# Performance work log

Measured on AMD Instinct MI355X. Metric: run time of the kernel, lower is better.

Reference implementation:

```python
import jax, jax.numpy as jnp
import numpy as np

N = 50000   # nodes
E = 300000  # directed edges (~Delaunay mesh, degree 6)
H = 128     # hidden_size
TW = 5      # time_window
P = 3       # process_steps
NODE_IN = 9
EDGE_IN = 4
LN_EPS = 1e-5


def _ln(x, g, b):
    m = jnp.mean(x, axis=-1, keepdims=True)
    v = jnp.var(x, axis=-1, keepdims=True)
    return (x - m) * jax.lax.rsqrt(v + LN_EPS) * g + b


def _mlp_ln(x, w1, b1, w2, b2, g, bb):
    # Linear -> ReLU -> Linear -> LayerNorm (matches MLP(..., layer_norm=True))
    h = jax.nn.relu(x @ w1 + b1)
    return _ln(h @ w2 + b2, g, bb)


def setup_inputs() -> dict:
    key = jax.random.key(0)
    ks = iter(jax.random.split(key, 64))
    def nrm(shape):
        return jax.random.normal(next(ks), shape, jnp.float32)
    def lin(fi, fo, stack=None):
        sh = (fi, fo) if stack is None else (stack, fi, fo)
        return nrm(sh) / np.sqrt(fi)
    inp = {}
    inp["temperature"] = nrm((N,))
    inp["temperature_prev"] = nrm((N,))
    inp["heat_source"] = nrm((N,))
    inp["heat_source_prev"] = nrm((N,))
    inp["heat_source_next"] = nrm((N, TW))
    inp["mesh_pos"] = jax.random.uniform(next(ks), (N, 2), jnp.float32)
    inp["edge_index"] = jax.random.randint(next(ks), (2, E), 0, N, jnp.int32)
    # Normalizer params (running mean/std)
    inp["node_norm_mean"] = jnp.zeros((NODE_IN,), jnp.float32)
    inp["node_norm_std"] = jnp.ones((NODE_IN,), jnp.float32)
    inp["edge_norm_mean"] = jnp.zeros((EDGE_IN,), jnp.float32)
    inp["edge_norm_std"] = jnp.ones((EDGE_IN,), jnp.float32)
    # node encoder
    inp["ne_w1"] = lin(NODE_IN, H); inp["ne_b1"] = jnp.zeros((H,), jnp.float32)
    inp["ne_w2"] = lin(H, H);       inp["ne_b2"] = jnp.zeros((H,), jnp.float32)
    inp["ne_g"] = jnp.ones((H,), jnp.float32); inp["ne_be"] = jnp.zeros((H,), jnp.float32)
    # edge encoder
    inp["ee_w1"] = lin(EDGE_IN, H); inp["ee_b1"] = jnp.zeros((H,), jnp.float32)
    inp["ee_w2"] = lin(H, H);       inp["ee_b2"] = jnp.zeros((H,), jnp.float32)
    inp["ee_g"] = jnp.ones((H,), jnp.float32); inp["ee_be"] = jnp.zeros((H,), jnp.float32)
    # processors (stacked over P steps): edge_mlp in=3H, node_mlp in=2H
    inp["pe_w1"] = lin(3 * H, H, P); inp["pe_b1"] = jnp.zeros((P, H), jnp.float32)
    inp["pe_w2"] = lin(H, H, P);     inp["pe_b2"] = jnp.zeros((P, H), jnp.float32)
    inp["pe_g"] = jnp.ones((P, H), jnp.float32); inp["pe_be"] = jnp.zeros((P, H), jnp.float32)
    inp["pn_w1"] = lin(2 * H, H, P); inp["pn_b1"] = jnp.zeros((P, H), jnp.float32)
    inp["pn_w2"] = lin(H, H, P);     inp["pn_b2"] = jnp.zeros((P, H), jnp.float32)
    inp["pn_g"] = jnp.ones((P, H), jnp.float32); inp["pn_be"] = jnp.zeros((P, H), jnp.float32)
    # decoder (Conv1d kernel_size=1 == per-node Linear), Swish in between
    inp["dec_w1"] = lin(H, H // 2); inp["dec_b1"] = jnp.zeros((H // 2,), jnp.float32)
    inp["dec_w2"] = lin(H // 2, TW); inp["dec_b2"] = jnp.zeros((TW,), jnp.float32)
    return inp


def reference(temperature, temperature_prev, heat_source, heat_source_prev,
              heat_source_next, mesh_pos, edge_index,
              node_norm_mean, node_norm_std, edge_norm_mean, edge_norm_std,
              ne_w1, ne_b1, ne_w2, ne_b2, ne_g, ne_be,
              ee_w1, ee_b1, ee_w2, ee_b2, ee_g, ee_be,
              pe_w1, pe_b1, pe_w2, pe_b2, pe_g, pe_be,
              pn_w1, pn_b1, pn_w2, pn_b2, pn_g, pn_be,
              dec_w1, dec_b1, dec_w2, dec_b2):
    u = temperature
    # node features: [u, u_dot, q, q_dot, q_next]  -> [N, 9]
    x = jnp.concatenate([
        u[:, None], (u - temperature_prev)[:, None],
        heat_source[:, None], (heat_source - heat_source_prev)[:, None],
        heat_source_next], axis=-1)
    s, r = edge_index[0], edge_index[1]  # senders (source j), receivers (target i)
    rel = mesh_pos[s] - mesh_pos[r]                       # [E, 2]
    dist = jnp.linalg.norm(rel, axis=-1, keepdims=True)   # [E, 1]
    relt = (u[s] - u[r])[:, None]                         # [E, 1]
    e = jnp.concatenate([rel, dist, relt], axis=-1)       # [E, 4]

    xh = _mlp_ln((x - node_norm_mean) / node_norm_std, ne_w1, ne_b1, ne_w2, ne_b2, ne_g, ne_be)
    eh = _mlp_ln((e - edge_norm_mean) / edge_norm_std, ee_w1, ee_b1, ee_w2, ee_b2, ee_g, ee_be)

    n_nodes = xh.shape[0]
    for i in range(P):
        xs, xr = xh[s], xh[r]  # x_j = x[source], x_i = x[target]
        # message: edge_mlp(cat[x_i, x_j, e]) then scatter-add at target index
        msg = _mlp_ln(jnp.concatenate([xr, xs, eh], axis=-1),
                      pe_w1[i], pe_b1[i], pe_w2[i], pe_b2[i], pe_g[i], pe_be[i])
        aggr = jax.ops.segment_sum(msg, r, num_segments=n_nodes)
        # node update + residual
        new_x = _mlp_ln(jnp.concatenate([aggr, xh], axis=-1),
                        pn_w1[i], pn_b1[i], pn_w2[i], pn_b2[i], pn_g[i], pn_be[i]) + xh
        # edge update (note row/col ordering differs from message) + residual
        new_e = _mlp_ln(jnp.concatenate([xs, xr, eh], axis=-1),
                        pe_w1[i], pe_b1[i], pe_w2[i], pe_b2[i], pe_g[i], pe_be[i]) + eh
        xh, eh = new_x, new_e

    # decoder: 1x1 convs == per-node linears, Swish(beta=1) activation
    h = xh @ dec_w1 + dec_b1
    h = h * jax.nn.sigmoid(h)
    delta = (h @ dec_w2 + dec_b2).reshape(-1, TW)
    dt = jnp.arange(1, TW + 1, dtype=delta.dtype)
    return dt[None, :] * delta
```

## Files before the change

### kernel.cpp

```cpp
#include <hip/hip_runtime.h>
#include <stdint.h>

typedef unsigned short u16;
typedef __attribute__((ext_vector_type(8))) short bf16x8_t;
typedef __attribute__((ext_vector_type(4))) float f32x4_t;

__device__ __forceinline__ float bl(u16 x) {
  union { unsigned u; float f; } c; c.u = ((unsigned)x) << 16; return c.f;
}
__device__ __forceinline__ u16 fb(float x) {
  union { float f; unsigned u; } c; c.f = x;
  unsigned r = c.u + 0x7fffu + ((c.u >> 16) & 1u);
  return (u16)(r >> 16);
}

__global__ void sentinel_kernel(float* out, int n) {
  int i = blockIdx.x * 256 + threadIdx.x;
  if (i < n) out[i] = 12345.f;
}

struct TSeg { const float* src; u16* dst; };
struct TArgs { TSeg s[23]; };
__global__ void transpose_w(TArgs a) {
  __shared__ u16 sT[128][132];
  const float* src = a.s[blockIdx.x].src;
  u16* dst = a.s[blockIdx.x].dst;
  for (int e = threadIdx.x; e < 16384; e += 256) {
    int k = e >> 7, n = e & 127;
    sT[n][k] = fb(src[e]);
  }
  __syncthreads();
  for (int e = threadIdx.x; e < 16384; e += 256) {
    int n = e >> 7, k = e & 127;
    dst[e] = sT[n][k];
  }
}

__global__ void zero_i32(int* p, int n) {
  int i = blockIdx.x * 256 + threadIdx.x;
  if (i < n) p[i] = 0;
}
__global__ void deg_count(const int* __restrict__ ei, int* __restrict__ cnt, int E) {
  int e = blockIdx.x * 256 + threadIdx.x;
  if (e < E) atomicAdd(&cnt[ei[E + e]], 1);
}
__global__ void scan1(const int* __restrict__ cnt, int* __restrict__ part,
                      int* __restrict__ bsum, int N) {
  __shared__ int s[256];
  int i = blockIdx.x * 256 + threadIdx.x;
  s[threadIdx.x] = (i < N) ? cnt[i] : 0;
  __syncthreads();
#pragma unroll
  for (int o = 1; o < 256; o <<= 1) {
    int t = (threadIdx.x >= o) ? s[threadIdx.x - o] : 0;
    __syncthreads();
    s[threadIdx.x] += t;
    __syncthreads();
  }
  if (i < N) part[i] = s[threadIdx.x];
  if (threadIdx.x == 255) bsum[blockIdx.x] = s[255];
}
__global__ void scan2(int* bsum, int nb) {
  __shared__ int s[256];
  __shared__ int carry;
  if (threadIdx.x == 0) carry = 0;
  __syncthreads();
  for (int base = 0; base < nb; base += 256) {
    int i = base + threadIdx.x;
    int v = (i < nb) ? bsum[i] : 0;
    s[threadIdx.x] = v;
    __syncthreads();
#pragma unroll
    for (int o = 1; o < 256; o <<= 1) {
      int t = (threadIdx.x >= o) ? s[threadIdx.x - o] : 0;
      __syncthreads();
      s[threadIdx.x] += t;
      __syncthreads();
    }
    int exc = s[threadIdx.x] - v + carry;
    if (i < nb) bsum[i] = exc;
    __syncthreads();
    if (threadIdx.x == 255) carry += s[255];
    __syncthreads();
  }
}
__global__ void scan3(const int* __restrict__ part, const int* __restrict__ bsum,
                      int* __restrict__ start, int N) {
  int i = blockIdx.x * 256 + threadIdx.x;
  if (i < N) start[i + 1] = part[i] + bsum[i >> 8];
  if (i == 0) start[0] = 0;
}
__global__ void fill_slot(const int* __restrict__ ei, int* __restrict__ cnt2,
                          const int* __restrict__ start, int* __restrict__ sortedS,
                          int* __restrict__ sortedR, int E) {
  int e = blockIdx.x * 256 + threadIdx.x;
  if (e >= E) return;
  int s = ei[e], r = ei[E + e];
  int p = atomicAdd(&cnt2[r], 1);
  int slot = start[r] + p;
  sortedS[slot] = s;
  sortedR[slot] = r;
}

__global__ void node_feat_kernel(const float* __restrict__ t, const float* __restrict__ tp,
                                 const float* __restrict__ q, const float* __restrict__ qp,
                                 const float* __restrict__ qn, const float* __restrict__ nm,
                                 const float* __restrict__ ns, float* __restrict__ nfeat,
                                 int n_nodes) {
  int n = blockIdx.x * 256 + threadIdx.x;
  if (n >= n_nodes) return;
  float u = t[n];
  float x[9];
  x[0] = u; x[1] = u - tp[n];
  float hq = q[n];
  x[2] = hq; x[3] = hq - qp[n];
#pragma unroll
  for (int j = 0; j < 5; ++j) x[4 + j] = qn[n * 5 + j];
#pragma unroll
  for (int k = 0; k < 9; ++k) nfeat[n * 9 + k] = (x[k] - nm[k]) / ns[k];
}

__global__ void edge_feat_kernel(const int* __restrict__ sArr, const int* __restrict__ rArr,
                                 const float* __restrict__ mp, const float* __restrict__ u,
                                 const float* __restrict__ em, const float* __restrict__ es,
                                 float* __restrict__ efeat, int n_edges) {
  int e = blockIdx.x * 256 + threadIdx.x;
  if (e >= n_edges) return;
  int s = sArr[e], r = rArr[e];
  float rx = mp[s * 2] - mp[r * 2];
  float ry = mp[s * 2 + 1] - mp[r * 2 + 1];
  float d = sqrtf(rx * rx + ry * ry);
  float rt = u[s] - u[r];
  float x[4] = {rx, ry, d, rt};
#pragma unroll
  for (int k = 0; k < 4; ++k) efeat[e * 4 + k] = (x[k] - em[k]) / es[k];
}

template <int K>
__global__ __launch_bounds__(256, 2) void encode_fused(
    const float* __restrict__ feat, const float* __restrict__ w1f, const float* __restrict__ b1f,
    const u16* __restrict__ wt2, const float* __restrict__ b2, const float* __restrict__ gg,
    const float* __restrict__ bb, u16* __restrict__ out, int M) {
  __shared__ float sW1[K * 128];
  __shared__ float sB1[128];
  __shared__ u16 sH[64][136];
  const int tid = threadIdx.x;
  const int wave = tid >> 6, lane = tid & 63;
  const int q = lane >> 4, l16 = lane & 15;
  const int m0 = blockIdx.x * 64;
  const int rowb = wave * 16 + q * 4;
  const int arow = m0 + wave * 16 + l16;
  const int arc = arow < M ? arow : M - 1;

  for (int i = tid; i < K * 128; i += 256) sW1[i] = w1f[i];
  if (tid < 128) sB1[tid] = b1f[tid];
  __syncthreads();

  float fr[K];
#pragma unroll
  for (int k = 0; k < K; ++k) fr[k] = feat[(size_t)arc * K + k];

  f32x4_t acc[8];
#pragma unroll
  for (int b = 0; b < 8; ++b) acc[b] = (f32x4_t){0.f, 0.f, 0.f, 0.f};
#pragma unroll
  for (int kk = 0; kk < 4; ++kk) {
    union { u16 u[8]; bf16x8_t v; } cv;
#pragma unroll
    for (int j = 0; j < 8; ++j) {
      int col = kk * 32 + q * 8 + j;
      float h = sB1[col];
#pragma unroll
      for (int k = 0; k < K; ++k) h += fr[k] * sW1[k * 128 + col];
      cv.u[j] = fb(h > 0.f ? h : 0.f);
    }
#pragma unroll
    for (int nt = 0; nt < 8; ++nt) {
      bf16x8_t bfv = *(const bf16x8_t*)(wt2 + (size_t)(nt * 16 + l16) * 128 + kk * 32 + q * 8);
      acc[nt] = __builtin_amdgcn_mfma_f32_16x16x32_bf16(cv.v, bfv, acc[nt], 0, 0, 0);
    }
  }

  float bcol[8], gcol[8], becol[8];
#pragma unroll
  for (int nt = 0; nt < 8; ++nt) {
    bcol[nt] = b2[nt * 16 + l16];
    gcol[nt] = gg[nt * 16 + l16];
    becol[nt] = bb[nt * 16 + l16];
  }
  float s[4] = {0, 0, 0, 0}, ss[4] = {0, 0, 0, 0};
#pragma unroll
  for (int r = 0; r < 4; ++r)
#pragma unroll
    for (int nt = 0; nt < 8; ++nt) {
      float v = acc[nt][r] + bcol[nt];
      s[r] += v;
      ss[r] += v * v;
    }
#pragma unroll
  for (int r = 0; r < 4; ++r) {
#pragma unroll
    for (int m = 1; m <= 8; m <<= 1) {
      s[r] += __shfl_xor(s[r], m, 64);
      ss[r] += __shfl_xor(ss[r], m, 64);
    }
  }
#pragma unroll
  for (int r = 0; r < 4; ++r) {
    float mean = s[r] * (1.f / 128.f);
    float var = fmaxf(ss[r] * (1.f / 128.f) - mean * mean, 0.f);
    float rstd = rsqrtf(var + 1e-5f);
#pragma unroll
    for (int nt = 0; nt < 8; ++nt) {
      float v = (acc[nt][r] + bcol[nt] - mean) * rstd * gcol[nt] + becol[nt];
      sH[rowb + r][nt * 16 + l16] = fb(v);
    }
  }
  __syncthreads();
#pragma unroll
  for (int it = 0; it < 4; ++it) {
    int lin = it * 256 + tid;
    int row = lin >> 4, ch = (lin & 15) * 8;
    int grow = m0 + row;
    if (grow >= M) continue;
    *(uint4*)(out + (size_t)grow * 128 + ch) = *(uint4*)(&sH[row][ch]);
  }
}

__global__ __launch_bounds__(256, 2) void gemm64_2w(
    const u16* __restrict__ A, const u16* __restrict__ WT0, const u16* __restrict__ WT1,
    u16* __restrict__ out0, u16* __restrict__ out1, float* __restrict__ aggr, int M) {
  __shared__ u16 sO0[64][136];
  __shared__ u16 sO1[64][136];
  const int tid = threadIdx.x;
  const int wave = tid >> 6, lane = tid & 63;
  const int q = lane >> 4, l16 = lane & 15;
  const int m0 = blockIdx.x * 64;
  int arow = m0 + wave * 16 + l16;
  if (arow >= M) arow = M - 1;

  {
    float4 z = make_float4(0.f, 0.f, 0.f, 0.f);
#pragma unroll
    for (int it = 0; it < 8; ++it) {
      int lin = it * 256 + tid;
      int row = lin >> 5, c4 = (lin & 31) * 4;
      int grow = m0 + row;
      if (grow < M) *(float4*)(aggr + (size_t)grow * 128 + c4) = z;
    }
  }

  f32x4_t a0[8], a1[8];
#pragma unroll
  for (int b = 0; b < 8; ++b) {
    a0[b] = (f32x4_t){0.f, 0.f, 0.f, 0.f};
    a1[b] = (f32x4_t){0.f, 0.f, 0.f, 0.f};
  }
#pragma unroll 2
  for (int kk = 0; kk < 4; ++kk) {
    bf16x8_t af = *(const bf16x8_t*)(A + (size_t)arow * 128 + kk * 32 + q * 8);
#pragma unroll
    for (int nt = 0; nt < 8; ++nt) {
      bf16x8_t b0 = *(const bf16x8_t*)(WT0 + (size_t)(nt * 16 + l16) * 128 + kk * 32 + q * 8);
      bf16x8_t b1v = *(const bf16x8_t*)(WT1 + (size_t)(nt * 16 + l16) * 128 + kk * 32 + q * 8);
      a0[nt] = __builtin_amdgcn_mfma_f32_16x16x32_bf16(af, b0, a0[nt], 0, 0, 0);
      a1[nt] = __builtin_amdgcn_mfma_f32_16x16x32_bf16(af, b1v, a1[nt], 0, 0, 0);
    }
  }
  const int rowb = wave * 16 + q * 4;
#pragma unroll
  for (int r = 0; r < 4; ++r)
#pragma unroll
    for (int nt = 0; nt < 8; ++nt) {
      sO0[rowb + r][nt * 16 + l16] = fb(a0[nt][r]);
      sO1[rowb + r][nt * 16 + l16] = fb(a1[nt][r]);
    }
  __syncthreads();
#pragma unroll
  for (int it = 0; it < 4; ++it) {
    int lin = it * 256 + tid;
    int row = lin >> 4, ch = (lin & 15) * 8;
    int grow = m0 + row;
    if (grow >= M) continue;
    *(uint4*)(out0 + (size_t)grow * 128 + ch) = *(uint4*)(&sO0[row][ch]);
    *(uint4*)(out1 + (size_t)grow * 128 + ch) = *(uint4*)(&sO1[row][ch]);
  }
}

__global__ __launch_bounds__(256, 2) void node_fused_2w(
    u16* __restrict__ xh, float* __restrict__ aggr, const u16* __restrict__ wtA,
    const u16* __restrict__ wtB, const float* __restrict__ b1, const u16* __restrict__ wt2,
    const float* __restrict__ b2, const float* __restrict__ gg, const float* __restrict__ bb,
    const u16* __restrict__ wtA2, const u16* __restrict__ wtB2, u16* __restrict__ xhA,
    u16* __restrict__ xhB, int M) {
  __shared__ u16 sH[64][136];
  __shared__ u16 sO1[64][136];
  const int tid = threadIdx.x;
  const int wave = tid >> 6, lane = tid & 63;
  const int q = lane >> 4, l16 = lane & 15;
  const int m0 = blockIdx.x * 64;
  const int rowb = wave * 16 + q * 4;
  const int arow = m0 + wave * 16 + l16;
  const int arc = arow < M ? arow : M - 1;

  bf16x8_t xf[4], af_[4];
#pragma unroll
  for (int kk = 0; kk < 4; ++kk) {
    xf[kk] = *(const bf16x8_t*)(xh + (size_t)arc * 128 + kk * 32 + q * 8);
    const float* ap = aggr + (size_t)arc * 128 + kk * 32 + q * 8;
    union { u16 u[8]; bf16x8_t v; } cv;
#pragma unroll
    for (int j = 0; j < 8; ++j) cv.u[j] = fb(ap[j]);
    af_[kk] = cv.v;
  }

  f32x4_t acc[8];
#pragma unroll
  for (int b = 0; b < 8; ++b) acc[b] = (f32x4_t){0.f, 0.f, 0.f, 0.f};
#pragma unroll
  for (int kk = 0; kk < 4; ++kk) {
#pragma unroll
    for (int nt = 0; nt < 8; ++nt) {
      bf16x8_t bA = *(const bf16x8_t*)(wtA + (size_t)(nt * 16 + l16) * 128 + kk * 32 + q * 8);
      bf16x8_t bB = *(const bf16x8_t*)(wtB + (size_t)(nt * 16 + l16) * 128 + kk * 32 + q * 8);
      acc[nt] = __builtin_amdgcn_mfma_f32_16x16x32_bf16(af_[kk], bA, acc[nt], 0, 0, 0);
      acc[nt] = __builtin_amdgcn_mfma_f32_16x16x32_bf16(xf[kk], bB, acc[nt], 0, 0, 0);
    }
  }
  float bcol1[8];
#pragma unroll
  for (int nt = 0; nt < 8; ++nt) bcol1[nt] = b1[nt * 16 + l16];
#pragma unroll
  for (int r = 0; r < 4; ++r)
#pragma unroll
    for (int nt = 0; nt < 8; ++nt) {
      float v = acc[nt][r] + bcol1[nt];
      sH[rowb + r][nt * 16 + l16] = fb(v > 0.f ? v : 0.f);
    }
  __syncthreads();

  f32x4_t acc2[8];
#pragma unroll
  for (int b = 0; b < 8; ++b) acc2[b] = (f32x4_t){0.f, 0.f, 0.f, 0.f};
#pragma unroll
  for (int kk = 0; kk < 4; ++kk) {
    bf16x8_t afm = *(const bf16x8_t*)(&sH[wave * 16 + l16][kk * 32 + q * 8]);
#pragma unroll
    for (int nt = 0; nt < 8; ++nt) {
      bf16x8_t bfv = *(const bf16x8_t*)(wt2 + (size_t)(nt * 16 + l16) * 128 + kk * 32 + q * 8);
      acc2[nt] = __builtin_amdgcn_mfma_f32_16x16x32_bf16(afm, bfv, acc2[nt], 0, 0, 0);
    }
  }
  float bcol[8], gcol[8], becol[8];
#pragma unroll
  for (int nt = 0; nt < 8; ++nt) {
    bcol[nt] = b2[nt * 16 + l16];
    gcol[nt] = gg[nt * 16 + l16];
    becol[nt] = bb[nt * 16 + l16];
  }
  float s[4] = {0, 0, 0, 0}, ss[4] = {0, 0, 0, 0};
#pragma unroll
  for (int r = 0; r < 4; ++r)
#pragma unroll
    for (int nt = 0; nt < 8; ++nt) {
      float v = acc2[nt][r] + bcol[nt];
      s[r] += v;
      ss[r] += v * v;
    }
#pragma unroll
  for (int r = 0; r < 4; ++r) {
#pragma unroll
    for (int m = 1; m <= 8; m <<= 1) {
      s[r] += __shfl_xor(s[r], m, 64);
      ss[r] += __shfl_xor(ss[r], m, 64);
    }
  }
  __syncthreads();
#pragma unroll
  for (int r = 0; r < 4; ++r) {
    float mean = s[r] * (1.f / 128.f);
    float var = fmaxf(ss[r] * (1.f / 128.f) - mean * mean, 0.f);
    float rstd = rsqrtf(var + 1e-5f);
#pragma unroll
    for (int nt = 0; nt < 8; ++nt) {
      float v = (acc2[nt][r] + bcol[nt] - mean) * rstd * gcol[nt] + becol[nt];
      sH[rowb + r][nt * 16 + l16] = fb(v);
    }
  }
  __syncthreads();

  bf16x8_t nf[4];
#pragma unroll
  for (int kk = 0; kk < 4; ++kk) {
    u16 y8[8];
    *(uint4*)y8 = *(uint4*)(&sH[wave * 16 + l16][kk * 32 + q * 8]);
#pragma unroll
    for (int j = 0; j < 8; ++j) y8[j] = fb(bl(y8[j]) + bl((u16)xf[kk][j]));
    nf[kk] = *(bf16x8_t*)y8;
    if (arow < M)
      *(uint4*)(xh + (size_t)arow * 128 + kk * 32 + q * 8) = *(uint4*)y8;
  }

  if (wtA2 == nullptr) return;

  if (arow < M) {
    float4 z = make_float4(0.f, 0.f, 0.f, 0.f);
#pragma unroll
    for (int kk = 0; kk < 4; ++kk) {
      *(float4*)(aggr + (size_t)arow * 128 + kk * 32 + q * 8) = z;
      *(float4*)(aggr + (size_t)arow * 128 + kk * 32 + q * 8 + 4) = z;
    }
  }

  f32x4_t a0[8], a1[8];
#pragma unroll
  for (int b = 0; b < 8; ++b) {
    a0[b] = (f32x4_t){0.f, 0.f, 0.f, 0.f};
    a1[b] = (f32x4_t){0.f, 0.f, 0.f, 0.f};
  }
#pragma unroll
  for (int kk = 0; kk < 4; ++kk) {
#pragma unroll
    for (int nt = 0; nt < 8; ++nt) {
      bf16x8_t b0 = *(const bf16x8_t*)(wtA2 + (size_t)(nt * 16 + l16) * 128 + kk * 32 + q * 8);
      bf16x8_t b1v = *(const bf16x8_t*)(wtB2 + (size_t)(nt * 16 + l16) * 128 + kk * 32 + q * 8);
      a0[nt] = __builtin_amdgcn_mfma_f32_16x16x32_bf16(nf[kk], b0, a0[nt], 0, 0, 0);
      a1[nt] = __builtin_amdgcn_mfma_f32_16x16x32_bf16(nf[kk], b1v, a1[nt], 0, 0, 0);
    }
  }
  __syncthreads();
#pragma unroll
  for (int r = 0; r < 4; ++r)
#pragma unroll
    for (int nt = 0; nt < 8; ++nt) {
      sH[rowb + r][nt * 16 + l16] = fb(a0[nt][r]);
      sO1[rowb + r][nt * 16 + l16] = fb(a1[nt][r]);
    }
  __syncthreads();
#pragma unroll
  for (int it = 0; it < 4; ++it) {
    int lin = it * 256 + tid;
    int row = lin >> 4, ch = (lin & 15) * 8;
    int grow = m0 + row;
    if (grow >= M) continue;
    *(uint4*)(xhA + (size_t)grow * 128 + ch) = *(uint4*)(&sH[row][ch]);
    *(uint4*)(xhB + (size_t)grow * 128 + ch) = *(uint4*)(&sO1[row][ch]);
  }
}

template <bool CSR, bool LAST>
__global__ __launch_bounds__(256, 2) void edge_fused(
    u16* __restrict__ eh, const u16* __restrict__ xhA, const u16* __restrict__ xhB,
    const u16* __restrict__ wtC, const float* __restrict__ b1, const u16* __restrict__ wt2,
    const float* __restrict__ b2, const float* __restrict__ gg, const float* __restrict__ bb,
    const int* __restrict__ sArr, const int* __restrict__ rArr,
    const int* __restrict__ startp, float* __restrict__ aggr, int E) {
  __shared__ u16 sHm[64][136];
  __shared__ u16 sHe[LAST ? 1 : 64][136];
  __shared__ int sR[64];
  __shared__ float sB1[128];
  const int tid = threadIdx.x;
  const int wave = tid >> 6, lane = tid & 63;
  const int q = lane >> 4, l16 = lane & 15;
  const int m0 = blockIdx.x * 64;
  const int rowb = wave * 16 + q * 4;
  int arow = m0 + wave * 16 + l16;
  int arc = arow < E ? arow : E - 1;

  if (tid < 64) {
    int e = m0 + tid;
    sR[tid] = (e < E) ? rArr[e] : -1;
  }
  if (tid < 128) sB1[tid] = b1[tid];

  int psv[4], prv[4];
#pragma unroll
  for (int it = 0; it < 4; ++it) {
    int lin = it * 256 + tid;
    int ge = m0 + (lin >> 4);
    int gc = ge < E ? ge : E - 1;
    psv[it] = sArr[gc];
    prv[it] = rArr[gc];
  }

  bf16x8_t ehf[4];
#pragma unroll
  for (int kk = 0; kk < 4; ++kk)
    ehf[kk] = *(const bf16x8_t*)(eh + (size_t)arc * 128 + kk * 32 + q * 8);

  f32x4_t accC[8];
#pragma unroll
  for (int b = 0; b < 8; ++b) accC[b] = (f32x4_t){0.f, 0.f, 0.f, 0.f};
#pragma unroll
  for (int kk = 0; kk < 4; ++kk) {
#pragma unroll
    for (int nt = 0; nt < 8; ++nt) {
      bf16x8_t bfv = *(const bf16x8_t*)(wtC + (size_t)(nt * 16 + l16) * 128 + kk * 32 + q * 8);
      accC[nt] = __builtin_amdgcn_mfma_f32_16x16x32_bf16(ehf[kk], bfv, accC[nt], 0, 0, 0);
    }
  }
  __builtin_amdgcn_sched_barrier(0);

  uint4 pAr[4], pBs[4], pAs[4], pBr[4];
#pragma unroll
  for (int it = 0; it < 4; ++it) {
    int ch = ((it * 256 + tid) & 15) * 8;
    pAr[it] = *(const uint4*)(xhA + (size_t)prv[it] * 128 + ch);
    pBs[it] = *(const uint4*)(xhB + (size_t)psv[it] * 128 + ch);
    if constexpr (!LAST) {
      pAs[it] = *(const uint4*)(xhA + (size_t)psv[it] * 128 + ch);
      pBr[it] = *(const uint4*)(xhB + (size_t)prv[it] * 128 + ch);
    }
  }

#pragma unroll
  for (int r = 0; r < 4; ++r)
#pragma unroll
    for (int nt = 0; nt < 8; ++nt) sHm[rowb + r][nt * 16 + l16] = fb(accC[nt][r]);
  __syncthreads();

#pragma unroll
  for (int it = 0; it < 4; ++it) {
    int lin = it * 256 + tid;
    int row = lin >> 4, ch = (lin & 15) * 8;
    bool ok = (m0 + row) < E;
    u16 t8[8], ar[8], as_[8], br[8], bs[8], hm[8], he[8];
    *(uint4*)t8 = *(uint4*)(&sHm[row][ch]);
    *(uint4*)ar = pAr[it];
    *(uint4*)bs = pBs[it];
    if constexpr (!LAST) {
      *(uint4*)as_ = pAs[it];
      *(uint4*)br = pBr[it];
    }
#pragma unroll
    for (int j = 0; j < 8; ++j) {
      float t = bl(t8[j]) + sB1[ch + j];
      float vm = t + bl(ar[j]) + bl(bs[j]);
      hm[j] = (ok && vm > 0.f) ? fb(vm) : 0;
      if constexpr (!LAST) {
        float ve = t + bl(as_[j]) + bl(br[j]);
        he[j] = (ok && ve > 0.f) ? fb(ve) : 0;
      }
    }
    *(uint4*)(&sHm[row][ch]) = *(uint4*)hm;
    if constexpr (!LAST) *(uint4*)(&sHe[row][ch]) = *(uint4*)he;
  }
  __syncthreads();

  float bcol[8], gcol[8], becol[8];
#pragma unroll
  for (int nt = 0; nt < 8; ++nt) {
    bcol[nt] = b2[nt * 16 + l16];
    gcol[nt] = gg[nt * 16 + l16];
    becol[nt] = bb[nt * 16 + l16];
  }

  f32x4_t accM[8], accE[8];
#pragma unroll
  for (int b = 0; b < 8; ++b) {
    accM[b] = (f32x4_t){0.f, 0.f, 0.f, 0.f};
    accE[b] = (f32x4_t){0.f, 0.f, 0.f, 0.f};
  }
#pragma unroll
  for (int kk = 0; kk < 4; ++kk) {
    bf16x8_t afm = *(const bf16x8_t*)(&sHm[wave * 16 + l16][kk * 32 + q * 8]);
    bf16x8_t afe;
    if constexpr (!LAST) afe = *(const bf16x8_t*)(&sHe[wave * 16 + l16][kk * 32 + q * 8]);
#pragma unroll
    for (int nt = 0; nt < 8; ++nt) {
      bf16x8_t bfv = *(const bf16x8_t*)(wt2 + (size_t)(nt * 16 + l16) * 128 + kk * 32 + q * 8);
      accM[nt] = __builtin_amdgcn_mfma_f32_16x16x32_bf16(afm, bfv, accM[nt], 0, 0, 0);
      if constexpr (!LAST)
        accE[nt] = __builtin_amdgcn_mfma_f32_16x16x32_bf16(afe, bfv, accE[nt], 0, 0, 0);
    }
  }
  float sm[4] = {0, 0, 0, 0}, ssm[4] = {0, 0, 0, 0};
  float se[4] = {0, 0, 0, 0}, sse[4] = {0, 0, 0, 0};
#pragma unroll
  for (int r = 0; r < 4; ++r)
#pragma unroll
    for (int nt = 0; nt < 8; ++nt) {
      float vm = accM[nt][r] + bcol[nt];
      sm[r] += vm; ssm[r] += vm * vm;
      if constexpr (!LAST) {
        float ve = accE[nt][r] + bcol[nt];
        se[r] += ve; sse[r] += ve * ve;
      }
    }
#pragma unroll
  for (int r = 0; r < 4; ++r) {
#pragma unroll
    for (int m = 1; m <= 8; m <<= 1) {
      sm[r] += __shfl_xor(sm[r], m, 64);
      ssm[r] += __shfl_xor(ssm[r], m, 64);
      if constexpr (!LAST) {
        se[r] += __shfl_xor(se[r], m, 64);
        sse[r] += __shfl_xor(sse[r], m, 64);
      }
    }
  }

  if (!CSR) {
#pragma unroll
    for (int r = 0; r < 4; ++r) {
      int row = m0 + rowb + r;
      if (row >= E) continue;
      int rr = sR[rowb + r];
      float mean = sm[r] * (1.f / 128.f);
      float var = fmaxf(ssm[r] * (1.f / 128.f) - mean * mean, 0.f);
      float rstd = rsqrtf(var + 1e-5f);
#pragma unroll
      for (int nt = 0; nt < 8; ++nt) {
        float v = (accM[nt][r] + bcol[nt] - mean) * rstd * gcol[nt] + becol[nt];
        atomicAdd(&aggr[(size_t)rr * 128 + nt * 16 + l16], v);
      }
    }
  }

  __syncthreads();
#pragma unroll
  for (int r = 0; r < 4; ++r) {
    float meanM = sm[r] * (1.f / 128.f);
    float varM = fmaxf(ssm[r] * (1.f / 128.f) - meanM * meanM, 0.f);
    float rstdM = rsqrtf(varM + 1e-5f);
    if constexpr (!LAST) {
      float meanE = se[r] * (1.f / 128.f);
      float varE = fmaxf(sse[r] * (1.f / 128.f) - meanE * meanE, 0.f);
      float rstdE = rsqrtf(varE + 1e-5f);
#pragma unroll
      for (int nt = 0; nt < 8; ++nt) {
        float ve = (accE[nt][r] + bcol[nt] - meanE) * rstdE * gcol[nt] + becol[nt];
        sHe[rowb + r][nt * 16 + l16] = fb(ve);
      }
    }
    if (CSR) {
#pragma unroll
      for (int nt = 0; nt < 8; ++nt) {
        float vm = (accM[nt][r] + bcol[nt] - meanM) * rstdM * gcol[nt] + becol[nt];
        sHm[rowb + r][nt * 16 + l16] = fb(vm);
      }
    }
  }
  __syncthreads();

#pragma unroll
  for (int it = 0; it < 4; ++it) {
    int lin = it * 256 + tid;
    int row = lin >> 4, ch = (lin & 15) * 8;
    int grow = m0 + row;
    if (grow >= E) continue;
    if constexpr (!LAST) {
      u16 y8[8], e8[8];
      *(uint4*)y8 = *(uint4*)(&sHe[row][ch]);
      *(uint4*)e8 = *(const uint4*)(eh + (size_t)grow * 128 + ch);
#pragma unroll
      for (int j = 0; j < 8; ++j) y8[j] = fb(bl(y8[j]) + bl(e8[j]));
      *(uint4*)(eh + (size_t)grow * 128 + ch) = *(uint4*)y8;
    }

    if (CSR) {
      int rr = sR[row];
      if (rr < 0) continue;
      bool first = (row == 0) || (sR[row - 1] != rr);
      if (!first) continue;
      int gs = startp[rr], ge2 = startp[rr + 1];
      int le = ge2 - m0;
      if (le > 64) le = 64;
      float acc[8] = {0, 0, 0, 0, 0, 0, 0, 0};
      for (int i = row; i < le; ++i) {
        u16 m8[8];
        *(uint4*)m8 = *(uint4*)(&sHm[i][ch]);
#pragma unroll
        for (int j = 0; j < 8; ++j) acc[j] += bl(m8[j]);
      }
      if (gs >= m0 && ge2 <= m0 + 64) {
        *(float4*)(aggr + (size_t)rr * 128 + ch) = make_float4(acc[0], acc[1], acc[2], acc[3]);
        *(float4*)(aggr + (size_t)rr * 128 + ch + 4) =
            make_float4(acc[4], acc[5], acc[6], acc[7]);
      } else {
#pragma unroll
        for (int j = 0; j < 8; ++j) atomicAdd(&aggr[(size_t)rr * 128 + ch + j], acc[j]);
      }
    }
  }
}

__global__ void decoder_kernel(const u16* __restrict__ xh, const float* __restrict__ w1,
                               const float* __restrict__ b1, const float* __restrict__ w2,
                               const float* __restrict__ b2, float* __restrict__ out,
                               int n_nodes) {
  __shared__ float sx[4][128];
  int tid = threadIdx.x;
  int lw = tid >> 6, lane = tid & 63;
  int n0 = blockIdx.x * 4;
  for (int i = tid; i < 512; i += 256) {
    int nn = i >> 7, c = i & 127;
    int n = n0 + nn;
    sx[nn][c] = (n < n_nodes) ? bl(xh[(size_t)n * 128 + c]) : 0.f;
  }
  __syncthreads();
  int n = n0 + lw;
  float h = b1[lane];
#pragma unroll 16
  for (int k = 0; k < 128; ++k) h += sx[lw][k] * w1[k * 64 + lane];
  float hs = h * (1.f / (1.f + __expf(-h)));
  float d[5];
#pragma unroll
  for (int t = 0; t < 5; ++t) {
    float p = hs * w2[lane * 5 + t];
#pragma unroll
    for (int m = 1; m <= 32; m <<= 1) p += __shfl_xor(p, m, 64);
    d[t] = p;
  }
  if (lane == 0 && n < n_nodes) {
#pragma unroll
    for (int t = 0; t < 5; ++t)
      out[(size_t)n * 5 + t] = (float)(t + 1) * (d[t] + b2[t]);
  }
}

extern "C" void kernel_launch(void* const* d_in, const int* in_sizes, int n_in, void* d_out,
                              int out_size, void* d_ws, size_t ws_size, hipStream_t stream) {
  auto F = [&](int i) { return (const float*)d_in[i]; };
  const int* edge_index = (const int*)d_in[6];
  const int N_ = in_sizes[0];
  const int E_ = in_sizes[6] / 2;

  char* wsb = (char*)d_ws;
  size_t off = 0;
  auto alloc = [&](size_t bytes) -> char* {
    char* p = wsb + off;
    off += (bytes + 255) & ~(size_t)255;
    return p;
  };
  u16* xh = (u16*)alloc((size_t)N_ * 128 * 2);
  u16* xhA = (u16*)alloc((size_t)N_ * 128 * 2);
  u16* xhB = (u16*)alloc((size_t)N_ * 128 * 2);
  u16* ehP = (u16*)alloc((size_t)E_ * 128 * 2);
  float* aggr = (float*)alloc((size_t)N_ * 128 * 4);
  float* nfeat = (float*)xhA;
  float* efeat = (float*)xhB;
  u16* wne2T = (u16*)alloc(16384 * 2);
  u16* wee2T = (u16*)alloc(16384 * 2);
  u16* wpe1T = (u16*)alloc((size_t)9 * 16384 * 2);
  u16* wpe2T = (u16*)alloc((size_t)3 * 16384 * 2);
  u16* wpn1T = (u16*)alloc((size_t)6 * 16384 * 2);
  u16* wpn2T = (u16*)alloc((size_t)3 * 16384 * 2);

  const size_t base_off = off;
  int* startp = (int*)alloc((size_t)(N_ + 1) * 4);
  int* cntp = (int*)alloc((size_t)N_ * 4);
  int* partp = (int*)alloc((size_t)N_ * 4);
  int* bsump = (int*)alloc(((size_t)(N_ + 255) / 256) * 4 + 256);
  int* sortedS = (int*)alloc((size_t)E_ * 4);
  int* sortedR = (int*)alloc((size_t)E_ * 4);
  bool useCSR = (off <= ws_size);
  if (!useCSR) {
    off = base_off;
    if (off > ws_size) {
      sentinel_kernel<<<(out_size + 255) / 256, 256, 0, stream>>>((float*)d_out, out_size);
      return;
    }
  }

  TArgs ta;
  int ts = 0;
  ta.s[ts++] = {F(13), wne2T};
  ta.s[ts++] = {F(19), wee2T};
  for (int i = 0; i < 3; ++i)
    for (int b = 0; b < 3; ++b)
      ta.s[ts++] = {F(23) + (size_t)(i * 3 + b) * 16384, wpe1T + (size_t)(i * 3 + b) * 16384};
  for (int i = 0; i < 3; ++i) ta.s[ts++] = {F(25) + (size_t)i * 16384, wpe2T + (size_t)i * 16384};
  for (int i = 0; i < 3; ++i)
    for (int b = 0; b < 2; ++b)
      ta.s[ts++] = {F(29) + (size_t)(i * 2 + b) * 16384, wpn1T + (size_t)(i * 2 + b) * 16384};
  for (int i = 0; i < 3; ++i) ta.s[ts++] = {F(31) + (size_t)i * 16384, wpn2T + (size_t)i * 16384};

  const int tilesN = (N_ + 63) / 64;
  const int tilesE = (E_ + 63) / 64;
  const int nb = (N_ + 255) / 256;
  dim3 blk(256);

  transpose_w<<<23, blk, 0, stream>>>(ta);

  const int* sArr = edge_index;
  const int* rArr = edge_index + E_;
  if (useCSR) {
    zero_i32<<<(N_ + 255) / 256, blk, 0, stream>>>(cntp, N_);
    deg_count<<<(E_ + 255) / 256, blk, 0, stream>>>(edge_index, cntp, E_);
    scan1<<<nb, blk, 0, stream>>>(cntp, partp, bsump, N_);
    scan2<<<1, blk, 0, stream>>>(bsump, nb);
    scan3<<<nb, blk, 0, stream>>>(partp, bsump, startp, N_);
    zero_i32<<<(N_ + 255) / 256, blk, 0, stream>>>(cntp, N_);
    fill_slot<<<(E_ + 255) / 256, blk, 0, stream>>>(edge_index, cntp, startp, sortedS, sortedR,
                                                    E_);
    sArr = sortedS;
    rArr = sortedR;
  }

  node_feat_kernel<<<(N_ + 255) / 256, blk, 0, stream>>>(F(0), F(1), F(2), F(3), F(4), F(7),
                                                         F(8), nfeat, N_);
  encode_fused<9><<<tilesN, blk, 0, stream>>>(nfeat, F(11), F(12), wne2T, F(14), F(15), F(16),
                                              xh, N_);
  edge_feat_kernel<<<(E_ + 255) / 256, blk, 0, stream>>>(sArr, rArr, F(5), F(0), F(9), F(10),
                                                         efeat, E_);
  encode_fused<4><<<tilesE, blk, 0, stream>>>(efeat, F(17), F(18), wee2T, F(20), F(21), F(22),
                                              ehP, E_);

  for (int i = 0; i < 3; ++i) {
    const u16* wtA = wpe1T + (size_t)(i * 3 + 0) * 16384;
    const u16* wtB = wpe1T + (size_t)(i * 3 + 1) * 16384;
    const u16* wtC = wpe1T + (size_t)(i * 3 + 2) * 16384;
    const float* pb1 = F(24) + i * 128;
    const u16* wt2 = wpe2T + (size_t)i * 16384;
    const float* pb2 = F(26) + i * 128;
    const float* pg = F(27) + i * 128;
    const float* pbe = F(28) + i * 128;
    const u16* wtnA = wpn1T + (size_t)(i * 2 + 0) * 16384;
    const u16* wtnB = wpn1T + (size_t)(i * 2 + 1) * 16384;
    const float* nb1 = F(30) + i * 128;
    const u16* wtn2 = wpn2T + (size_t)i * 16384;
    const float* nb2 = F(32) + i * 128;
    const float* ng = F(33) + i * 128;
    const float* nbe = F(34) + i * 128;

    if (i == 0)
      gemm64_2w<<<tilesN, blk, 0, stream>>>(xh, wtA, wtB, xhA, xhB, aggr, N_);
    const bool last = (i == 2);
    if (useCSR) {
      if (last)
        edge_fused<true, true><<<tilesE, blk, 0, stream>>>(ehP, xhA, xhB, wtC, pb1, wt2, pb2,
                                                           pg, pbe, sArr, rArr, startp, aggr, E_);
      else
        edge_fused<true, false><<<tilesE, blk, 0, stream>>>(ehP, xhA, xhB, wtC, pb1, wt2, pb2,
                                                            pg, pbe, sArr, rArr, startp, aggr, E_);
    } else {
      if (last)
        edge_fused<false, true><<<tilesE, blk, 0, stream>>>(ehP, xhA, xhB, wtC, pb1, wt2, pb2,
                                                            pg, pbe, sArr, rArr, nullptr, aggr, E_);
      else
        edge_fused<false, false><<<tilesE, blk, 0, stream>>>(ehP, xhA, xhB, wtC, pb1, wt2, pb2,
                                                             pg, pbe, sArr, rArr, nullptr, aggr, E_);
    }
    const u16* wtA2 = (i < 2) ? wpe1T + (size_t)((i + 1) * 3 + 0) * 16384 : nullptr;
    const u16* wtB2 = (i < 2) ? wpe1T + (size_t)((i + 1) * 3 + 1) * 16384 : nullptr;
    node_fused_2w<<<tilesN, blk, 0, stream>>>(xh, aggr, wtnA, wtnB, nb1, wtn2, nb2, ng, nbe,
                                              wtA2, wtB2, xhA, xhB, N_);
  }

  decoder_kernel<<<(N_ + 3) / 4, blk, 0, stream>>>(xh, F(35), F(36), F(37), F(38),
                                                   (float*)d_out, N_);
}
```

Before: 1.165 ms.

## Split fused edge kernel into separate message and edge-update kernels for occupancy

```diff
diff --git a/kernel.cpp b/kernel.cpp
--- a/kernel.cpp
+++ b/kernel.cpp
@@ -448,144 +448,92 @@
   }
 }
 
-template <bool CSR, bool LAST>
-__global__ __launch_bounds__(256, 2) void edge_fused(
-    u16* __restrict__ eh, const u16* __restrict__ xhA, const u16* __restrict__ xhB,
+template <bool CSR>
+__global__ __launch_bounds__(256, 8) void msg_kernel(
+    const u16* __restrict__ eh, const u16* __restrict__ xhA, const u16* __restrict__ xhB,
     const u16* __restrict__ wtC, const float* __restrict__ b1, const u16* __restrict__ wt2,
     const float* __restrict__ b2, const float* __restrict__ gg, const float* __restrict__ bb,
     const int* __restrict__ sArr, const int* __restrict__ rArr,
     const int* __restrict__ startp, float* __restrict__ aggr, int E) {
   __shared__ u16 sHm[64][136];
-  __shared__ u16 sHe[LAST ? 1 : 64][136];
   __shared__ int sR[64];
-  __shared__ float sB1[128];
+  __shared__ float sB1[128], sB2[128], sG[128], sBe[128];
   const int tid = threadIdx.x;
   const int wave = tid >> 6, lane = tid & 63;
   const int q = lane >> 4, l16 = lane & 15;
   const int m0 = blockIdx.x * 64;
   const int rowb = wave * 16 + q * 4;
-  int arow = m0 + wave * 16 + l16;
-  int arc = arow < E ? arow : E - 1;
-
-  if (tid < 64) {
-    int e = m0 + tid;
-    sR[tid] = (e < E) ? rArr[e] : -1;
-  }
-  if (tid < 128) sB1[tid] = b1[tid];
-
-  int psv[4], prv[4];
-#pragma unroll
-  for (int it = 0; it < 4; ++it) {
-    int lin = it * 256 + tid;
-    int ge = m0 + (lin >> 4);
-    int gc = ge < E ? ge : E - 1;
-    psv[it] = sArr[gc];
-    prv[it] = rArr[gc];
-  }
-
-  bf16x8_t ehf[4];
-#pragma unroll
-  for (int kk = 0; kk < 4; ++kk)
-    ehf[kk] = *(const bf16x8_t*)(eh + (size_t)arc * 128 + kk * 32 + q * 8);
-
-  f32x4_t accC[8];
-#pragma unroll
-  for (int b = 0; b < 8; ++b) accC[b] = (f32x4_t){0.f, 0.f, 0.f, 0.f};
-#pragma unroll
-  for (int kk = 0; kk < 4; ++kk) {
+  const int arow = m0 + wave * 16 + l16;
+  const int arc = arow < E ? arow : E - 1;
+
+  if (tid < 64) sR[tid] = (m0 + tid < E) ? rArr[m0 + tid] : -1;
+  if (tid < 128) {
+    sB1[tid] = b1[tid]; sB2[tid] = b2[tid]; sG[tid] = gg[tid]; sBe[tid] = bb[tid];
+  }
+
+  f32x4_t acc[8];
+#pragma unroll
+  for (int b = 0; b < 8; ++b) acc[b] = (f32x4_t){0.f, 0.f, 0.f, 0.f};
+#pragma unroll
+  for (int kk = 0; kk < 4; ++kk) {
+    bf16x8_t ef = *(const bf16x8_t*)(eh + (size_t)arc * 128 + kk * 32 + q * 8);
 #pragma unroll
     for (int nt = 0; nt < 8; ++nt) {
       bf16x8_t bfv = *(const bf16x8_t*)(wtC + (size_t)(nt * 16 + l16) * 128 + kk * 32 + q * 8);
-      accC[nt] = __builtin_amdgcn_mfma_f32_16x16x32_bf16(ehf[kk], bfv, accC[nt], 0, 0, 0);
-    }
-  }
-  __builtin_amdgcn_sched_barrier(0);
-
-  uint4 pAr[4], pBs[4], pAs[4], pBr[4];
-#pragma unroll
-  for (int it = 0; it < 4; ++it) {
-    int ch = ((it * 256 + tid) & 15) * 8;
-    pAr[it] = *(const uint4*)(xhA + (size_t)prv[it] * 128 + ch);
-    pBs[it] = *(const uint4*)(xhB + (size_t)psv[it] * 128 + ch);
-    if constexpr (!LAST) {
-      pAs[it] = *(const uint4*)(xhA + (size_t)psv[it] * 128 + ch);
-      pBr[it] = *(const uint4*)(xhB + (size_t)prv[it] * 128 + ch);
-    }
-  }
-
+      acc[nt] = __builtin_amdgcn_mfma_f32_16x16x32_bf16(ef, bfv, acc[nt], 0, 0, 0);
+    }
+  }
 #pragma unroll
   for (int r = 0; r < 4; ++r)
 #pragma unroll
-    for (int nt = 0; nt < 8; ++nt) sHm[rowb + r][nt * 16 + l16] = fb(accC[nt][r]);
-  __syncthreads();
-
-#pragma unroll
+    for (int nt = 0; nt < 8; ++nt) sHm[rowb + r][nt * 16 + l16] = fb(acc[nt][r]);
+  __syncthreads();
+
+#pragma unroll 2
   for (int it = 0; it < 4; ++it) {
     int lin = it * 256 + tid;
     int row = lin >> 4, ch = (lin & 15) * 8;
-    bool ok = (m0 + row) < E;
-    u16 t8[8], ar[8], as_[8], br[8], bs[8], hm[8], he[8];
+    int ge = m0 + row;
+    int gc = ge < E ? ge : E - 1;
+    int ps = sArr[gc], pr = rArr[gc];
+    uint4 av = *(const uint4*)(xhA + (size_t)pr * 128 + ch);
+    uint4 bv = *(const uint4*)(xhB + (size_t)ps * 128 + ch);
+    bool ok = ge < E;
+    u16 t8[8], ar[8], bs[8], hm[8];
     *(uint4*)t8 = *(uint4*)(&sHm[row][ch]);
-    *(uint4*)ar = pAr[it];
-    *(uint4*)bs = pBs[it];
-    if constexpr (!LAST) {
-      *(uint4*)as_ = pAs[it];
-      *(uint4*)br = pBr[it];
-    }
+    *(uint4*)ar = av;
+    *(uint4*)bs = bv;
 #pragma unroll
     for (int j = 0; j < 8; ++j) {
-      float t = bl(t8[j]) + sB1[ch + j];
-      float vm = t + bl(ar[j]) + bl(bs[j]);
-      hm[j] = (ok && vm > 0.f) ? fb(vm) : 0;
-      if constexpr (!LAST) {
-        float ve = t + bl(as_[j]) + bl(br[j]);
-        he[j] = (ok && ve > 0.f) ? fb(ve) : 0;
-      }
+      float v = bl(t8[j]) + sB1[ch + j] + bl(ar[j]) + bl(bs[j]);
+      hm[j] = (ok && v > 0.f) ? fb(v) : 0;
     }
     *(uint4*)(&sHm[row][ch]) = *(uint4*)hm;
-    if constexpr (!LAST) *(uint4*)(&sHe[row][ch]) = *(uint4*)he;
-  }
-  __syncthreads();
-
-  float bcol[8], gcol[8], becol[8];
-#pragma unroll
-  for (int nt = 0; nt < 8; ++nt) {
-    bcol[nt] = b2[nt * 16 + l16];
-    gcol[nt] = gg[nt * 16 + l16];
-    becol[nt] = bb[nt * 16 + l16];
-  }
-
-  f32x4_t accM[8], accE[8];
-#pragma unroll
-  for (int b = 0; b < 8; ++b) {
-    accM[b] = (f32x4_t){0.f, 0.f, 0.f, 0.f};
-    accE[b] = (f32x4_t){0.f, 0.f, 0.f, 0.f};
-  }
+  }
+  __syncthreads();
+
+#pragma unroll
+  for (int b = 0; b < 8; ++b) acc[b] = (f32x4_t){0.f, 0.f, 0.f, 0.f};
 #pragma unroll
   for (int kk = 0; kk < 4; ++kk) {
     bf16x8_t afm = *(const bf16x8_t*)(&sHm[wave * 16 + l16][kk * 32 + q * 8]);
-    bf16x8_t afe;
-    if constexpr (!LAST) afe = *(const bf16x8_t*)(&sHe[wave * 16 + l16][kk * 32 + q * 8]);
 #pragma unroll
     for (int nt = 0; nt < 8; ++nt) {
       bf16x8_t bfv = *(const bf16x8_t*)(wt2 + (size_t)(nt * 16 + l16) * 128 + kk * 32 + q * 8);
-      accM[nt] = __builtin_amdgcn_mfma_f32_16x16x32_bf16(afm, bfv, accM[nt], 0, 0, 0);
-      if constexpr (!LAST)
-        accE[nt] = __builtin_amdgcn_mfma_f32_16x16x32_bf16(afe, bfv, accE[nt], 0, 0, 0);
-    }
-  }
+      acc[nt] = __builtin_amdgcn_mfma_f32_16x16x32_bf16(afm, bfv, acc[nt], 0, 0, 0);
+    }
+  }
+  float bc[8];
+#pragma unroll
+  for (int nt = 0; nt < 8; ++nt) bc[nt] = sB2[nt * 16 + l16];
   float sm[4] = {0, 0, 0, 0}, ssm[4] = {0, 0, 0, 0};
-  float se[4] = {0, 0, 0, 0}, sse[4] = {0, 0, 0, 0};
 #pragma unroll
   for (int r = 0; r < 4; ++r)
 #pragma unroll
     for (int nt = 0; nt < 8; ++nt) {
-      float vm = accM[nt][r] + bcol[nt];
-      sm[r] += vm; ssm[r] += vm * vm;
-      if constexpr (!LAST) {
-        float ve = accE[nt][r] + bcol[nt];
-        se[r] += ve; sse[r] += ve * ve;
-      }
+      float v = acc[nt][r] + bc[nt];
+      sm[r] += v;
+      ssm[r] += v * v;
     }
 #pragma unroll
   for (int r = 0; r < 4; ++r) {
@@ -593,10 +541,6 @@
     for (int m = 1; m <= 8; m <<= 1) {
       sm[r] += __shfl_xor(sm[r], m, 64);
       ssm[r] += __shfl_xor(ssm[r], m, 64);
-      if constexpr (!LAST) {
-        se[r] += __shfl_xor(se[r], m, 64);
-        sse[r] += __shfl_xor(sse[r], m, 64);
-      }
     }
   }
 
@@ -611,34 +555,22 @@
       float rstd = rsqrtf(var + 1e-5f);
 #pragma unroll
       for (int nt = 0; nt < 8; ++nt) {
-        float v = (accM[nt][r] + bcol[nt] - mean) * rstd * gcol[nt] + becol[nt];
+        float v = (acc[nt][r] + bc[nt] - mean) * rstd * sG[nt * 16 + l16] + sBe[nt * 16 + l16];
         atomicAdd(&aggr[(size_t)rr * 128 + nt * 16 + l16], v);
       }
     }
-  }
-
-  __syncthreads();
+    return;
+  }
+
 #pragma unroll
   for (int r = 0; r < 4; ++r) {
-    float meanM = sm[r] * (1.f / 128.f);
-    float varM = fmaxf(ssm[r] * (1.f / 128.f) - meanM * meanM, 0.f);
-    float rstdM = rsqrtf(varM + 1e-5f);
-    if constexpr (!LAST) {
-      float meanE = se[r] * (1.f / 128.f);
-      float varE = fmaxf(sse[r] * (1.f / 128.f) - meanE * meanE, 0.f);
-      float rstdE = rsqrtf(varE + 1e-5f);
-#pragma unroll
-      for (int nt = 0; nt < 8; ++nt) {
-        float ve = (accE[nt][r] + bcol[nt] - meanE) * rstdE * gcol[nt] + becol[nt];
-        sHe[rowb + r][nt * 16 + l16] = fb(ve);
-      }
-    }
-    if (CSR) {
-#pragma unroll
-      for (int nt = 0; nt < 8; ++nt) {
-        float vm = (accM[nt][r] + bcol[nt] - meanM) * rstdM * gcol[nt] + becol[nt];
-        sHm[rowb + r][nt * 16 + l16] = fb(vm);
-      }
+    float mean = sm[r] * (1.f / 128.f);
+    float var = fmaxf(ssm[r] * (1.f / 128.f) - mean * mean, 0.f);
+    float rstd = rsqrtf(var + 1e-5f);
+#pragma unroll
+    for (int nt = 0; nt < 8; ++nt) {
+      float v = (acc[nt][r] + bc[nt] - mean) * rstd * sG[nt * 16 + l16] + sBe[nt * 16 + l16];
+      sHm[rowb + r][nt * 16 + l16] = fb(v);
     }
   }
   __syncthreads();
@@ -649,39 +581,147 @@
     int row = lin >> 4, ch = (lin & 15) * 8;
     int grow = m0 + row;
     if (grow >= E) continue;
-    if constexpr (!LAST) {
-      u16 y8[8], e8[8];
-      *(uint4*)y8 = *(uint4*)(&sHe[row][ch]);
-      *(uint4*)e8 = *(const uint4*)(eh + (size_t)grow * 128 + ch);
-#pragma unroll
-      for (int j = 0; j < 8; ++j) y8[j] = fb(bl(y8[j]) + bl(e8[j]));
-      *(uint4*)(eh + (size_t)grow * 128 + ch) = *(uint4*)y8;
-    }
-
-    if (CSR) {
-      int rr = sR[row];
-      if (rr < 0) continue;
-      bool first = (row == 0) || (sR[row - 1] != rr);
-      if (!first) continue;
-      int gs = startp[rr], ge2 = startp[rr + 1];
-      int le = ge2 - m0;
-      if (le > 64) le = 64;
-      float acc[8] = {0, 0, 0, 0, 0, 0, 0, 0};
-      for (int i = row; i < le; ++i) {
-        u16 m8[8];
-        *(uint4*)m8 = *(uint4*)(&sHm[i][ch]);
-#pragma unroll
-        for (int j = 0; j < 8; ++j) acc[j] += bl(m8[j]);
-      }
-      if (gs >= m0 && ge2 <= m0 + 64) {
-        *(float4*)(aggr + (size_t)rr * 128 + ch) = make_float4(acc[0], acc[1], acc[2], acc[3]);
-        *(float4*)(aggr + (size_t)rr * 128 + ch + 4) =
-            make_float4(acc[4], acc[5], acc[6], acc[7]);
-      } else {
-#pragma unroll
-        for (int j = 0; j < 8; ++j) atomicAdd(&aggr[(size_t)rr * 128 + ch + j], acc[j]);
-      }
-    }
+    int rr = sR[row];
+    if (rr < 0) continue;
+    bool first = (row == 0) || (sR[row - 1] != rr);
+    if (!first) continue;
+    int gs = startp[rr], ge2 = startp[rr + 1];
+    int le = ge2 - m0;
+    if (le > 64) le = 64;
+    float acc8[8] = {0, 0, 0, 0, 0, 0, 0, 0};
+    for (int i = row; i < le; ++i) {
+      u16 m8[8];
+      *(uint4*)m8 = *(uint4*)(&sHm[i][ch]);
+#pragma unroll
+      for (int j = 0; j < 8; ++j) acc8[j] += bl(m8[j]);
+    }
+    if (gs >= m0 && ge2 <= m0 + 64) {
+      *(float4*)(aggr + (size_t)rr * 128 + ch) = make_float4(acc8[0], acc8[1], acc8[2], acc8[3]);
+      *(float4*)(aggr + (size_t)rr * 128 + ch + 4) =
+          make_float4(acc8[4], acc8[5], acc8[6], acc8[7]);
+    } else {
+#pragma unroll
+      for (int j = 0; j < 8; ++j) atomicAdd(&aggr[(size_t)rr * 128 + ch + j], acc8[j]);
+    }
+  }
+}
+
+__global__ __launch_bounds__(256, 8) void edgeupd_kernel(
+    u16* __restrict__ eh, const u16* __restrict__ xhA, const u16* __restrict__ xhB,
+    const u16* __restrict__ wtC, const float* __restrict__ b1, const u16* __restrict__ wt2,
+    const float* __restrict__ b2, const float* __restrict__ gg, const float* __restrict__ bb,
+    const int* __restrict__ sArr, const int* __restrict__ rArr, int E) {
+  __shared__ u16 sHe[64][136];
+  __shared__ float sB1[128], sB2[128], sG[128], sBe[128];
+  const int tid = threadIdx.x;
+  const int wave = tid >> 6, lane = tid & 63;
+  const int q = lane >> 4, l16 = lane & 15;
+  const int m0 = blockIdx.x * 64;
+  const int rowb = wave * 16 + q * 4;
+  const int arow = m0 + wave * 16 + l16;
+  const int arc = arow < E ? arow : E - 1;
+
+  if (tid < 128) {
+    sB1[tid] = b1[tid]; sB2[tid] = b2[tid]; sG[tid] = gg[tid]; sBe[tid] = bb[tid];
+  }
+
+  f32x4_t acc[8];
+#pragma unroll
+  for (int b = 0; b < 8; ++b) acc[b] = (f32x4_t){0.f, 0.f, 0.f, 0.f};
+#pragma unroll
+  for (int kk = 0; kk < 4; ++kk) {
+    bf16x8_t ef = *(const bf16x8_t*)(eh + (size_t)arc * 128 + kk * 32 + q * 8);
+#pragma unroll
+    for (int nt = 0; nt < 8; ++nt) {
+      bf16x8_t bfv = *(const bf16x8_t*)(wtC + (size_t)(nt * 16 + l16) * 128 + kk * 32 + q * 8);
+      acc[nt] = __builtin_amdgcn_mfma_f32_16x16x32_bf16(ef, bfv, acc[nt], 0, 0, 0);
+    }
+  }
+#pragma unroll
+  for (int r = 0; r < 4; ++r)
+#pragma unroll
+    for (int nt = 0; nt < 8; ++nt) sHe[rowb + r][nt * 16 + l16] = fb(acc[nt][r]);
+  __syncthreads();
+
+#pragma unroll 2
+  for (int it = 0; it < 4; ++it) {
+    int lin = it * 256 + tid;
+    int row = lin >> 4, ch = (lin & 15) * 8;
+    int ge = m0 + row;
+    int gc = ge < E ? ge : E - 1;
+    int ps = sArr[gc], pr = rArr[gc];
+    uint4 av = *(const uint4*)(xhA + (size_t)ps * 128 + ch);
+    uint4 bv = *(const uint4*)(xhB + (size_t)pr * 128 + ch);
+    bool ok = ge < E;
+    u16 t8[8], as_[8], br[8], he[8];
+    *(uint4*)t8 = *(uint4*)(&sHe[row][ch]);
+    *(uint4*)as_ = av;
+    *(uint4*)br = bv;
+#pragma unroll
+    for (int j = 0; j < 8; ++j) {
+      float v = bl(t8[j]) + sB1[ch + j] + bl(as_[j]) + bl(br[j]);
+      he[j] = (ok && v > 0.f) ? fb(v) : 0;
+    }
+    *(uint4*)(&sHe[row][ch]) = *(uint4*)he;
+  }
+  __syncthreads();
+
+#pragma unroll
+  for (int b = 0; b < 8; ++b) acc[b] = (f32x4_t){0.f, 0.f, 0.f, 0.f};
+#pragma unroll
+  for (int kk = 0; kk < 4; ++kk) {
+    bf16x8_t afe = *(const bf16x8_t*)(&sHe[wave * 16 + l16][kk * 32 + q * 8]);
+#pragma unroll
+    for (int nt = 0; nt < 8; ++nt) {
+      bf16x8_t bfv = *(const bf16x8_t*)(wt2 + (size_t)(nt * 16 + l16) * 128 + kk * 32 + q * 8);
+      acc[nt] = __builtin_amdgcn_mfma_f32_16x16x32_bf16(afe, bfv, acc[nt], 0, 0, 0);
+    }
+  }
+  float bc[8];
+#pragma unroll
+  for (int nt = 0; nt < 8; ++nt) bc[nt] = sB2[nt * 16 + l16];
+  float se[4] = {0, 0, 0, 0}, sse[4] = {0, 0, 0, 0};
+#pragma unroll
+  for (int r = 0; r < 4; ++r)
+#pragma unroll
+    for (int nt = 0; nt < 8; ++nt) {
+      float v = acc[nt][r] + bc[nt];
+      se[r] += v;
+      sse[r] += v * v;
+    }
+#pragma unroll
+  for (int r = 0; r < 4; ++r) {
+#pragma unroll
+    for (int m = 1; m <= 8; m <<= 1) {
+      se[r] += __shfl_xor(se[r], m, 64);
+      sse[r] += __shfl_xor(sse[r], m, 64);
+    }
+  }
+#pragma unroll
+  for (int r = 0; r < 4; ++r) {
+    float mean = se[r] * (1.f / 128.f);
+    float var = fmaxf(sse[r] * (1.f / 128.f) - mean * mean, 0.f);
+    float rstd = rsqrtf(var + 1e-5f);
+#pragma unroll
+    for (int nt = 0; nt < 8; ++nt) {
+      float v = (acc[nt][r] + bc[nt] - mean) * rstd * sG[nt * 16 + l16] + sBe[nt * 16 + l16];
+      sHe[rowb + r][nt * 16 + l16] = fb(v);
+    }
+  }
+  __syncthreads();
+
+#pragma unroll
+  for (int it = 0; it < 4; ++it) {
+    int lin = it * 256 + tid;
+    int row = lin >> 4, ch = (lin & 15) * 8;
+    int grow = m0 + row;
+    if (grow >= E) continue;
+    u16 y8[8], e8[8];
+    *(uint4*)y8 = *(uint4*)(&sHe[row][ch]);
+    *(uint4*)e8 = *(const uint4*)(eh + (size_t)grow * 128 + ch);
+#pragma unroll
+    for (int j = 0; j < 8; ++j) y8[j] = fb(bl(y8[j]) + bl(e8[j]));
+    *(uint4*)(eh + (size_t)grow * 128 + ch) = *(uint4*)y8;
   }
 }
 
@@ -826,22 +866,18 @@
 
     if (i == 0)
       gemm64_2w<<<tilesN, blk, 0, stream>>>(xh, wtA, wtB, xhA, xhB, aggr, N_);
-    const bool last = (i == 2);
-    if (useCSR) {
-      if (last)
-        edge_fused<true, true><<<tilesE, blk, 0, stream>>>(ehP, xhA, xhB, wtC, pb1, wt2, pb2,
-                                                           pg, pbe, sArr, rArr, startp, aggr, E_);
-      else
-        edge_fused<true, false><<<tilesE, blk, 0, stream>>>(ehP, xhA, xhB, wtC, pb1, wt2, pb2,
-                                                            pg, pbe, sArr, rArr, startp, aggr, E_);
-    } else {
-      if (last)
-        edge_fused<false, true><<<tilesE, blk, 0, stream>>>(ehP, xhA, xhB, wtC, pb1, wt2, pb2,
-                                                            pg, pbe, sArr, rArr, nullptr, aggr, E_);
-      else
-        edge_fused<false, false><<<tilesE, blk, 0, stream>>>(ehP, xhA, xhB, wtC, pb1, wt2, pb2,
-                                                             pg, pbe, sArr, rArr, nullptr, aggr, E_);
-    }
+
+    if (useCSR)
+      msg_kernel<true><<<tilesE, blk, 0, stream>>>(ehP, xhA, xhB, wtC, pb1, wt2, pb2, pg, pbe,
+                                                   sArr, rArr, startp, aggr, E_);
+    else
+      msg_kernel<false><<<tilesE, blk, 0, stream>>>(ehP, xhA, xhB, wtC, pb1, wt2, pb2, pg, pbe,
+                                                    sArr, rArr, nullptr, aggr, E_);
+
+    if (i < 2)
+      edgeupd_kernel<<<tilesE, blk, 0, stream>>>(ehP, xhA, xhB, wtC, pb1, wt2, pb2, pg, pbe,
+                                                 sArr, rArr, E_);
+
     const u16* wtA2 = (i < 2) ? wpe1T + (size_t)((i + 1) * 3 + 0) * 16384 : nullptr;
     const u16* wtB2 = (i < 2) ? wpe1T + (size_t)((i + 1) * 3 + 1) * 16384 : nullptr;
     node_fused_2w<<<tilesN, blk, 0, stream>>>(xh, aggr, wtnA, wtnB, nb1, wtn2, nb2, ng, nbe,
```

Result: slower. 1.642 ms (+41.0%).
